# Kernel tuning notes

Measured on AMD Instinct MI355X. Metric: run time of the kernel, lower is better.

Reference implementation:

```python
import jax, jax.numpy as jnp
import numpy as np

D_MODEL = 128; N_HEADS = 8; N_LEVELS = 1; N_POINTS = 8
MAX_RES = 10.0
B, H_SP, W_SP = 8, 64, 64


def setup_inputs() -> dict:
    key = jax.random.key(0)
    ks = jax.random.split(key, 8)
    s = 0.02
    f32 = jnp.float32
    return {
        "nbr_fea": jax.random.normal(ks[0], (B, D_MODEL, H_SP, W_SP), f32),
        "ext_fea": jax.random.normal(ks[1], (B, D_MODEL, H_SP, W_SP), f32),
        "W_val": jax.random.normal(ks[2], (D_MODEL, D_MODEL), f32) * s,
        "b_val": jnp.zeros((D_MODEL,), f32),
        "W_off": jax.random.normal(ks[3], (D_MODEL, N_HEADS * N_LEVELS * N_POINTS * 2), f32) * s,
        "b_off": jax.random.normal(ks[4], (N_HEADS * N_LEVELS * N_POINTS * 2,), f32) * s,
        "W_attn": jax.random.normal(ks[5], (D_MODEL, N_HEADS * N_LEVELS * N_POINTS), f32) * s,
        "b_attn": jnp.zeros((N_HEADS * N_LEVELS * N_POINTS,), f32),
        "W_out": jax.random.normal(ks[6], (D_MODEL, D_MODEL), f32) * s,
        "b_out": jnp.zeros((D_MODEL,), f32),
    }


def _deform_attn_align(nbr_fea, ext_fea, W_val, b_val, W_off, b_off, W_attn, b_attn, W_out, b_out):
    b, c, h, w = nbr_fea.shape
    L = h * w
    dh = c // N_HEADS
    # flatten b c h w -> b (h w) c
    query = jnp.transpose(ext_fea, (0, 2, 3, 1)).reshape(b, L, c)
    vin = jnp.transpose(nbr_fea, (0, 2, 3, 1)).reshape(b, L, c)

    # value projection (mask is all-False -> no masked fill needed)
    value = (vin @ W_val + b_val).reshape(b, L, N_HEADS, dh)
    vh = jnp.transpose(value, (0, 2, 1, 3))  # [b, H, L, dh]

    # sampling offsets, clamped by max_residue_magnitude * tanh
    off = MAX_RES * jnp.tanh(query @ W_off + b_off)
    off = off.reshape(b, L, N_HEADS, N_POINTS, 2)  # single level
    attn = jax.nn.softmax((query @ W_attn + b_attn).reshape(b, L, N_HEADS, N_POINTS), axis=-1)

    # reference points in [0,1]; valid_ratio == 1 since padding mask is all-False
    yy, xx = jnp.meshgrid(jnp.arange(h, dtype=jnp.float32), jnp.arange(w, dtype=jnp.float32), indexing="ij")
    ref = jnp.stack([(xx.reshape(-1) + 0.5) / w, (yy.reshape(-1) + 0.5) / h], axis=-1)  # [L, 2]
    norm = jnp.array([w, h], jnp.float32)  # offset_normalizer [W, H]
    loc = ref[None, :, None, None, :] + off / norm  # [b, L, H, P, 2]

    # grid_sample(align_corners=False, padding_mode='zeros') pixel coordinates
    px = jnp.transpose(loc[..., 0] * w - 0.5, (0, 2, 1, 3))  # [b, H, L, P]
    py = jnp.transpose(loc[..., 1] * h - 0.5, (0, 2, 1, 3))

    x0 = jnp.floor(px); y0 = jnp.floor(py)
    fx = px - x0; fy = py - y0
    x0i = x0.astype(jnp.int32); y0i = y0.astype(jnp.int32)

    def gather(xi, yi):
        valid = (xi >= 0) & (xi < w) & (yi >= 0) & (yi < h)
        idx = jnp.clip(yi, 0, h - 1) * w + jnp.clip(xi, 0, w - 1)  # [b, H, L, P]
        g = jnp.take_along_axis(vh, idx.reshape(b, N_HEADS, L * N_POINTS)[..., None], axis=2)
        return g.reshape(b, N_HEADS, L, N_POINTS, dh) * valid[..., None]

    samp = (gather(x0i, y0i) * ((1.0 - fx) * (1.0 - fy))[..., None]
            + gather(x0i + 1, y0i) * (fx * (1.0 - fy))[..., None]
            + gather(x0i, y0i + 1) * ((1.0 - fx) * fy)[..., None]
            + gather(x0i + 1, y0i + 1) * (fx * fy)[..., None])  # [b, H, L, P, dh]

    aw = jnp.transpose(attn, (0, 2, 1, 3))  # [b, H, L, P]
    out = jnp.sum(samp * aw[..., None], axis=3)  # [b, H, L, dh]
    out = jnp.transpose(out, (0, 2, 1, 3)).reshape(b, L, c)
    out = out @ W_out + b_out
    return jnp.transpose(out.reshape(b, h, w, c), (0, 3, 1, 2))  # b c h w


def reference(nbr_fea, ext_fea, W_val, b_val, W_off, b_off, W_attn, b_attn, W_out, b_out):
    return _deform_attn_align(nbr_fea, ext_fea, W_val, b_val, W_off, b_off, W_attn, b_attn, W_out, b_out)
```

## Files before the change

kernel.cpp:

```cpp
#include <hip/hip_runtime.h>
#include <cstdint>

#define HB 8
#define CM 128
#define NHEAD 8
#define NPT 8
#define DHD 16
#define HS 64
#define WS 64
#define LTOT 4096
#define NQA 192
#define QAP 196
#define LFP 132
#define WPP 33

typedef float floatx4 __attribute__((ext_vector_type(4)));
typedef short bf16x8 __attribute__((ext_vector_type(8)));

__device__ __forceinline__ unsigned short f2bf_rne(float x) {
  unsigned u = __float_as_uint(x);
  return (unsigned short)((u + 0x7FFFu + ((u >> 16) & 1)) >> 16);
}
__device__ __forceinline__ void split_bf(float x, unsigned short& h, unsigned short& l) {
  unsigned u = __float_as_uint(x);
  h = (unsigned short)(u >> 16);
  float r = x - __uint_as_float(u & 0xFFFF0000u);
  l = (unsigned short)(__float_as_uint(r) >> 16);
}
__device__ __forceinline__ float fast_tanh(float x) {
  float e = __expf(2.0f * x);
  return 1.0f - 2.0f / (e + 1.0f);
}
__device__ __forceinline__ void bf8_fma(floatx4& oa, floatx4& ob, const uint4 r, const float wc) {
  floatx4 va = {__uint_as_float(r.x << 16), __uint_as_float(r.x & 0xFFFF0000u),
                __uint_as_float(r.y << 16), __uint_as_float(r.y & 0xFFFF0000u)};
  floatx4 vb = {__uint_as_float(r.z << 16), __uint_as_float(r.z & 0xFFFF0000u),
                __uint_as_float(r.w << 16), __uint_as_float(r.w & 0xFFFF0000u)};
  oa += va * wc;
  ob += vb * wc;
}

__global__ __launch_bounds__(256) void prep(const float* __restrict__ Wv,
                                            const float* __restrict__ Wo,
                                            const float* __restrict__ Wa,
                                            const float* __restrict__ Ww,
                                            const float* __restrict__ bo,
                                            const float* __restrict__ ba,
                                            unsigned short* __restrict__ wf_val,
                                            unsigned short* __restrict__ wf_qa,
                                            unsigned short* __restrict__ wf_out,
                                            float* __restrict__ bias_qa) {
  const int gid = blockIdx.x * 256 + threadIdx.x;
  const int k4 = gid / 448;
  const int ng = gid - k4 * 448;

  const float* src;
  unsigned short* dst;
  int Nsrc, Nn, nd, n;
  if (ng < 128) {        src = Wv; dst = wf_val; Nsrc = 128; Nn = 128; n = ng;        nd = n; }
  else if (ng < 256) {   src = Wo; dst = wf_qa;  Nsrc = 128; Nn = 192; n = ng - 128;  nd = n; }
  else if (ng < 320) {   src = Wa; dst = wf_qa;  Nsrc = 64;  Nn = 192; n = ng - 256;  nd = n + 128; }
  else {                 src = Ww; dst = wf_out; Nsrc = 128; Nn = 128; n = ng - 320;  nd = n; }

  ushort4 hi, lo;
  split_bf(src[(k4 * 4 + 0) * Nsrc + n], hi.x, lo.x);
  split_bf(src[(k4 * 4 + 1) * Nsrc + n], hi.y, lo.y);
  split_bf(src[(k4 * 4 + 2) * Nsrc + n], hi.z, lo.z);
  split_bf(src[(k4 * 4 + 3) * Nsrc + n], hi.w, lo.w);
  const int off = (k4 >> 1) * Nn * 8 + nd * 8 + (k4 & 1) * 4;
  *(ushort4*)(dst + off) = hi;
  *(ushort4*)(dst + Nn * 128 + off) = lo;

  if (gid < 128) bias_qa[gid] = bo[gid];
  else if (gid < 192) bias_qa[gid] = ba[gid - 128];
}

__global__ __launch_bounds__(256, 4) void gemm_val(const float* __restrict__ nbr,
                                                   const unsigned short* __restrict__ WF,
                                                   const float* __restrict__ bias,
                                                   unsigned short* __restrict__ value) {
  __shared__ __align__(16) char smem[33792];
  unsigned short* AB = (unsigned short*)smem;
  const int t = threadIdx.x;
  const int ml0 = blockIdx.x * 64;
  const int b = blockIdx.y;

  {
    const float* src = nbr + (size_t)b * CM * LTOT + ml0;
    const int x = t & 63, kq = t >> 6;
#pragma unroll
    for (int i = 0; i < 8; i++) {
      const int kb = kq * 4 + i * 16;
      ushort4 hi, lo;
      split_bf(src[(size_t)(kb + 0) * LTOT + x], hi.x, lo.x);
      split_bf(src[(size_t)(kb + 1) * LTOT + x], hi.y, lo.y);
      split_bf(src[(size_t)(kb + 2) * LTOT + x], hi.z, lo.z);
      split_bf(src[(size_t)(kb + 3) * LTOT + x], hi.w, lo.w);
      const int off = x * 128 + (((kb >> 3) ^ (x & 15)) << 3) + (kb & 7);
      *(ushort4*)(AB + off) = hi;
      *(ushort4*)(AB + 8192 + off) = lo;
    }
  }
  __syncthreads();

  const int w = t >> 6, lane = t & 63;
  const int wm = (w >> 1) * 32, wn = (w & 1) * 64;
  const int nl = lane & 15, q = lane >> 4;

  floatx4 acc[2][4];
#pragma unroll
  for (int mt = 0; mt < 2; mt++)
#pragma unroll
    for (int j = 0; j < 4; j++) acc[mt][j] = {0.0f, 0.0f, 0.0f, 0.0f};

#pragma unroll
  for (int K0 = 0; K0 < 4; K0++) {
    bf16x8 ah[2], al[2];
#pragma unroll
    for (int mt = 0; mt < 2; mt++) {
      const int m = wm + mt * 16 + nl;
      const int off = m * 128 + (((K0 * 4 + q) ^ (m & 15)) << 3);
      ah[mt] = *(bf16x8*)(AB + off);
      al[mt] = *(bf16x8*)(AB + 8192 + off);
    }
#pragma unroll
    for (int j = 0; j < 4; j++) {
      const size_t o = (size_t)(K0 * 4 + q) * CM * 8 + (wn + j * 16 + nl) * 8;
      const bf16x8 wh = *(const bf16x8*)(WF + o);
      const bf16x8 wl = *(const bf16x8*)(WF + (size_t)CM * 128 + o);
#pragma unroll
      for (int mt = 0; mt < 2; mt++) {
        acc[mt][j] = __builtin_amdgcn_mfma_f32_16x16x32_bf16(al[mt], wh, acc[mt][j], 0, 0, 0);
        acc[mt][j] = __builtin_amdgcn_mfma_f32_16x16x32_bf16(ah[mt], wl, acc[mt][j], 0, 0, 0);
        acc[mt][j] = __builtin_amdgcn_mfma_f32_16x16x32_bf16(ah[mt], wh, acc[mt][j], 0, 0, 0);
      }
    }
  }

  __syncthreads();
  float* LF = (float*)smem;
#pragma unroll
  for (int j = 0; j < 4; j++) {
    const int gc = wn + j * 16 + nl;
    const float bv = bias[gc];
#pragma unroll
    for (int mt = 0; mt < 2; mt++)
#pragma unroll
      for (int r = 0; r < 4; r++)
        LF[(wm + mt * 16 + q * 4 + r) * LFP + gc] = acc[mt][j][r] + bv;
  }
  __syncthreads();
#pragma unroll
  for (int i = 0; i < 4; i++) {
    const int c = t + i * 256;
    const int h = c >> 7, rem = c & 127, l = rem >> 1, half = rem & 1;
    const float* sp = LF + l * LFP + h * 16 + half * 8;
    uint4 st;
    st.x = ((unsigned)f2bf_rne(sp[1]) << 16) | f2bf_rne(sp[0]);
    st.y = ((unsigned)f2bf_rne(sp[3]) << 16) | f2bf_rne(sp[2]);
    st.z = ((unsigned)f2bf_rne(sp[5]) << 16) | f2bf_rne(sp[4]);
    st.w = ((unsigned)f2bf_rne(sp[7]) << 16) | f2bf_rne(sp[6]);
    *(uint4*)(value + ((size_t)(b * NHEAD + h) * LTOT + ml0 + l) * DHD + half * 8) = st;
  }
}

__global__ __launch_bounds__(256, 2) void samp(const float* __restrict__ ext,
                                               const unsigned short* __restrict__ value,
                                               const unsigned short* __restrict__ wf_qa,
                                               const unsigned short* __restrict__ wf_out,
                                               const float* __restrict__ bias_qa,
                                               const float* __restrict__ b_out,
                                               float* __restrict__ out) {
  __shared__ __align__(16) char smem[33792];
  unsigned short* AB = (unsigned short*)smem;
  float* qaT = (float*)smem;
  float2* WXY = (float2*)smem;
  float* WA = (float*)(smem + 16896);
  unsigned short* FR = (unsigned short*)(smem + 25344);

  const int t = threadIdx.x;
  const int b = blockIdx.x & 7;
  const int ml0 = (blockIdx.x >> 3) * 32;
  const int w = t >> 6, lane = t & 63;
  const int nl = lane & 15, q = lane >> 4;

  {
    const float* src = ext + (size_t)b * CM * LTOT + ml0;
    const int x = t & 31, kq = t >> 5;
#pragma unroll
    for (int i = 0; i < 4; i++) {
      const int kb = i * 32 + kq * 4;
      ushort4 hi, lo;
      split_bf(src[(size_t)(kb + 0) * LTOT + x], hi.x, lo.x);
      split_bf(src[(size_t)(kb + 1) * LTOT + x], hi.y, lo.y);
      split_bf(src[(size_t)(kb + 2) * LTOT + x], hi.z, lo.z);
      split_bf(src[(size_t)(kb + 3) * LTOT + x], hi.w, lo.w);
      const int off = x * 128 + (((kb >> 3) ^ (x & 15)) << 3) + (kb & 7);
      *(ushort4*)(AB + off) = hi;
      *(ushort4*)(AB + 4096 + off) = lo;
    }
  }
  __syncthreads();

  {
    const int wm = (w & 1) * 16;
    const int wn = (w >> 1) * 96;
    floatx4 acc[6];
#pragma unroll
    for (int j = 0; j < 6; j++) acc[j] = {0.0f, 0.0f, 0.0f, 0.0f};
#pragma unroll
    for (int K0 = 0; K0 < 4; K0++) {
      const int m = wm + nl;
      const int off = m * 128 + (((K0 * 4 + q) ^ (m & 15)) << 3);
      const bf16x8 ah = *(bf16x8*)(AB + off);
      const bf16x8 al = *(bf16x8*)(AB + 4096 + off);
#pragma unroll
      for (int j = 0; j < 6; j++) {
        const size_t o = (size_t)(K0 * 4 + q) * NQA * 8 + (wn + j * 16 + nl) * 8;
        const bf16x8 wh = *(const bf16x8*)(wf_qa + o);
        const bf16x8 wl = *(const bf16x8*)(wf_qa + (size_t)NQA * 128 + o);
        acc[j] = __builtin_amdgcn_mfma_f32_16x16x32_bf16(al, wh, acc[j], 0, 0, 0);
        acc[j] = __builtin_amdgcn_mfma_f32_16x16x32_bf16(ah, wl, acc[j], 0, 0, 0);
        acc[j] = __builtin_amdgcn_mfma_f32_16x16x32_bf16(ah, wh, acc[j], 0, 0, 0);
      }
    }
    __syncthreads();
#pragma unroll
    for (int j = 0; j < 6; j++) {
      const int n = wn + j * 16 + nl;
      const float bv = bias_qa[n];
#pragma unroll
      for (int r = 0; r < 4; r++)
        qaT[(wm + q * 4 + r) * QAP + n] = acc[j][r] + bv;
    }
  }
  __syncthreads();

  {
    const int ll = t >> 3, h = t & 7;
    const float* qrow = qaT + ll * QAP;
    float4 of[4];
#pragma unroll
    for (int j = 0; j < 4; j++) of[j] = *(const float4*)(qrow + h * 16 + j * 4);
    const float4 lga = *(const float4*)(qrow + 128 + h * 8);
    const float4 lgb = *(const float4*)(qrow + 128 + h * 8 + 4);
    __syncthreads();
    const float lg[8] = {lga.x, lga.y, lga.z, lga.w, lgb.x, lgb.y, lgb.z, lgb.w};
    float m = lg[0];
#pragma unroll
    for (int p = 1; p < 8; p++) m = fmaxf(m, lg[p]);
    float e[8], s = 0.0f;
#pragma unroll
    for (int p = 0; p < 8; p++) { e[p] = __expf(lg[p] - m); s += e[p]; }
    const float inv = 1.0f / s;
    const int l = ml0 + ll;
    const float xf = (float)(l & (WS - 1));
    const float yf = (float)(l >> 6);
#pragma unroll
    for (int p = 0; p < 8; p++) {
      const float ox = (p & 1) ? of[p >> 1].z : of[p >> 1].x;
      const float oy = (p & 1) ? of[p >> 1].w : of[p >> 1].y;
      WXY[(h * 8 + p) * WPP + ll] = {xf + 10.0f * fast_tanh(ox), yf + 10.0f * fast_tanh(oy)};
      WA[(h * 8 + p) * WPP + ll] = e[p] * inv;
    }
  }
  __syncthreads();

  {
    const int llq = lane >> 1, half = lane & 1;
    const int llm = llq & 15;
#pragma unroll
    for (int hi2 = 0; hi2 < 2; hi2++) {
      const int hh = w + hi2 * 4;
      const unsigned short* vb = value + (size_t)(b * NHEAD + hh) * LTOT * DHD + half * 8;
      floatx4 oa = {0.f, 0.f, 0.f, 0.f}, ob = oa;
#pragma unroll
      for (int p = 0; p < 8; p++) {
        const float2 pxy = WXY[(hh * 8 + p) * WPP + llq];
        const float a = WA[(hh * 8 + p) * WPP + llq];
        const float x0f = floorf(pxy.x), y0f = floorf(pxy.y);
        const float fx = pxy.x - x0f, fy = pxy.y - y0f;
        const int ix = (int)x0f, iy = (int)y0f;
        float wc[4];
        unsigned adr[4];
#pragma unroll
        for (int c = 0; c < 4; c++) {
          const int cdx = c & 1, cdy = c >> 1;
          const int jx = ix + cdx, jy = iy + cdy;
          const float wx = cdx ? fx : 1.0f - fx;
          const float wy = cdy ? fy : 1.0f - fy;
          const bool valid = ((unsigned)jx < WS) & ((unsigned)jy < HS);
          wc[c] = valid ? a * wx * wy : 0.0f;
          const int cx = min(max(jx, 0), WS - 1);
          const int cy = min(max(jy, 0), HS - 1);
          adr[c] = (unsigned)((cy << 6) + cx) * DHD;
        }
        uint4 r[4];
#pragma unroll
        for (int c = 0; c < 4; c++) r[c] = *(const uint4*)(vb + adr[c]);
#pragma unroll
        for (int c = 0; c < 4; c++) bf8_fma(oa, ob, r[c], wc[c]);
      }
      const int off = llq * 128 + (((hh * 2 + half) ^ llm) << 3);
      uint4 st;
      st.x = ((unsigned)f2bf_rne(oa[1]) << 16) | f2bf_rne(oa[0]);
      st.y = ((unsigned)f2bf_rne(oa[3]) << 16) | f2bf_rne(oa[2]);
      st.z = ((unsigned)f2bf_rne(ob[1]) << 16) | f2bf_rne(ob[0]);
      st.w = ((unsigned)f2bf_rne(ob[3]) << 16) | f2bf_rne(ob[2]);
      *(uint4*)(FR + off) = st;
    }
  }
  __syncthreads();

  {
    const int wm = (w & 1) * 16;
    const int wn = (w >> 1) * 64;
    floatx4 acc[4];
#pragma unroll
    for (int j = 0; j < 4; j++) acc[j] = {0.0f, 0.0f, 0.0f, 0.0f};
#pragma unroll
    for (int K0 = 0; K0 < 4; K0++) {
      const int m = wm + nl;
      const int off = m * 128 + (((K0 * 4 + q) ^ (m & 15)) << 3);
      const bf16x8 ah = *(bf16x8*)(FR + off);
#pragma unroll
      for (int j = 0; j < 4; j++) {
        const int n = wn + j * 16 + nl;
        const size_t o = (size_t)(K0 * 4 + q) * CM * 8 + n * 8;
        const bf16x8 wh = *(const bf16x8*)(wf_out + o);
        const bf16x8 wl = *(const bf16x8*)(wf_out + (size_t)CM * 128 + o);
        acc[j] = __builtin_amdgcn_mfma_f32_16x16x32_bf16(ah, wl, acc[j], 0, 0, 0);
        acc[j] = __builtin_amdgcn_mfma_f32_16x16x32_bf16(ah, wh, acc[j], 0, 0, 0);
      }
    }
#pragma unroll
    for (int j = 0; j < 4; j++) {
      const int gc = wn + j * 16 + nl;
      const float bv = b_out[gc];
      float4 st = {acc[j][0] + bv, acc[j][1] + bv, acc[j][2] + bv, acc[j][3] + bv};
      *(float4*)(out + ((size_t)b * CM + gc) * LTOT + ml0 + wm + q * 4) = st;
    }
  }
}

extern "C" void kernel_launch(void* const* d_in, const int* in_sizes, int n_in,
                              void* d_out, int out_size, void* d_ws, size_t ws_size,
                              hipStream_t stream) {
  const float* nbr    = (const float*)d_in[0];
  const float* ext    = (const float*)d_in[1];
  const float* W_val  = (const float*)d_in[2];
  const float* b_val  = (const float*)d_in[3];
  const float* W_off  = (const float*)d_in[4];
  const float* b_off  = (const float*)d_in[5];
  const float* W_attn = (const float*)d_in[6];
  const float* b_attn = (const float*)d_in[7];
  const float* W_out  = (const float*)d_in[8];
  const float* b_out  = (const float*)d_in[9];
  float* out = (float*)d_out;

  unsigned short* value = (unsigned short*)d_ws;
  unsigned short* wf_val = value + (size_t)HB * NHEAD * LTOT * DHD;
  unsigned short* wf_qa  = wf_val + 128 * 128 * 2;
  unsigned short* wf_out = wf_qa + 192 * 128 * 2;
  float* bias_qa = (float*)(wf_out + 128 * 128 * 2);

  prep<<<56, 256, 0, stream>>>(W_val, W_off, W_attn, W_out, b_off, b_attn,
                               wf_val, wf_qa, wf_out, bias_qa);
  gemm_val<<<dim3(64, HB), 256, 0, stream>>>(nbr, wf_val, b_val, value);
  samp<<<dim3(128 * HB), 256, 0, stream>>>(ext, value, wf_qa, wf_out, bias_qa, b_out, out);
}
```

Baseline: 136.6 us.

## Move query projection into the value-projection kernel and slim the sampling kernel

The offset/attention projection, tanh and softmax move out of the sampling kernel into a combined projection kernel. That kernel runs 1024 value-projection blocks (now 32 rows each) alongside 1024 query-projection blocks. Sampling positions and weights are packed to a global buffer, so the sampling kernel needs only 8 KB of shared memory and can target occupancy 4 instead of 2. The cost is an extra global round trip of about 24 floats per (position, head), roughly 25 MB written and read back.

New measurement: 152.2 us. +11.4%, slower.

```diff
diff --git a/kernel.cpp b/kernel.cpp
--- a/kernel.cpp
+++ b/kernel.cpp
@@ -12,7 +12,6 @@
 #define NQA 192
 #define QAP 196
 #define LFP 132
-#define WPP 33
 
 typedef float floatx4 __attribute__((ext_vector_type(4)));
 typedef short bf16x8 __attribute__((ext_vector_type(8)));
@@ -75,108 +74,188 @@
   else if (gid < 192) bias_qa[gid] = ba[gid - 128];
 }
 
-__global__ __launch_bounds__(256, 4) void gemm_val(const float* __restrict__ nbr,
-                                                   const unsigned short* __restrict__ WF,
-                                                   const float* __restrict__ bias,
-                                                   unsigned short* __restrict__ value) {
-  __shared__ __align__(16) char smem[33792];
-  unsigned short* AB = (unsigned short*)smem;
+__global__ __launch_bounds__(256, 4) void proj(const float* __restrict__ nbr,
+                                               const float* __restrict__ ext,
+                                               const unsigned short* __restrict__ wf_val,
+                                               const float* __restrict__ b_val,
+                                               const unsigned short* __restrict__ wf_qa,
+                                               const float* __restrict__ bias_qa,
+                                               unsigned short* __restrict__ value,
+                                               float* __restrict__ wpack) {
+  __shared__ __align__(16) char smem[25088];
   const int t = threadIdx.x;
-  const int ml0 = blockIdx.x * 64;
-  const int b = blockIdx.y;
-
-  {
-    const float* src = nbr + (size_t)b * CM * LTOT + ml0;
-    const int x = t & 63, kq = t >> 6;
-#pragma unroll
-    for (int i = 0; i < 8; i++) {
-      const int kb = kq * 4 + i * 16;
-      ushort4 hi, lo;
-      split_bf(src[(size_t)(kb + 0) * LTOT + x], hi.x, lo.x);
-      split_bf(src[(size_t)(kb + 1) * LTOT + x], hi.y, lo.y);
-      split_bf(src[(size_t)(kb + 2) * LTOT + x], hi.z, lo.z);
-      split_bf(src[(size_t)(kb + 3) * LTOT + x], hi.w, lo.w);
-      const int off = x * 128 + (((kb >> 3) ^ (x & 15)) << 3) + (kb & 7);
-      *(ushort4*)(AB + off) = hi;
-      *(ushort4*)(AB + 8192 + off) = lo;
+  const int w = t >> 6, lane = t & 63;
+  const int nl = lane & 15, q = lane >> 4;
+
+  if (blockIdx.x < 1024) {
+    const int bx = blockIdx.x;
+    const int b = bx >> 7;
+    const int ml0 = (bx & 127) * 32;
+    unsigned short* AB = (unsigned short*)smem;
+    {
+      const float* src = nbr + (size_t)b * CM * LTOT + ml0;
+      const int x = t & 31, kq = t >> 5;
+#pragma unroll
+      for (int i = 0; i < 4; i++) {
+        const int kb = i * 32 + kq * 4;
+        ushort4 hi, lo;
+        split_bf(src[(size_t)(kb + 0) * LTOT + x], hi.x, lo.x);
+        split_bf(src[(size_t)(kb + 1) * LTOT + x], hi.y, lo.y);
+        split_bf(src[(size_t)(kb + 2) * LTOT + x], hi.z, lo.z);
+        split_bf(src[(size_t)(kb + 3) * LTOT + x], hi.w, lo.w);
+        const int off = x * 128 + (((kb >> 3) ^ (x & 15)) << 3) + (kb & 7);
+        *(ushort4*)(AB + off) = hi;
+        *(ushort4*)(AB + 4096 + off) = lo;
+      }
+    }
+    __syncthreads();
+
+    const int wm = (w & 1) * 16, wn = (w >> 1) * 64;
+    floatx4 acc[4];
+#pragma unroll
+    for (int j = 0; j < 4; j++) acc[j] = {0.0f, 0.0f, 0.0f, 0.0f};
+
+#pragma unroll
+    for (int K0 = 0; K0 < 4; K0++) {
+      const int m = wm + nl;
+      const int off = m * 128 + (((K0 * 4 + q) ^ (m & 15)) << 3);
+      const bf16x8 ah = *(bf16x8*)(AB + off);
+      const bf16x8 al = *(bf16x8*)(AB + 4096 + off);
+#pragma unroll
+      for (int j = 0; j < 4; j++) {
+        const size_t o = (size_t)(K0 * 4 + q) * CM * 8 + (wn + j * 16 + nl) * 8;
+        const bf16x8 wh = *(const bf16x8*)(wf_val + o);
+        const bf16x8 wl = *(const bf16x8*)(wf_val + (size_t)CM * 128 + o);
+        acc[j] = __builtin_amdgcn_mfma_f32_16x16x32_bf16(al, wh, acc[j], 0, 0, 0);
+        acc[j] = __builtin_amdgcn_mfma_f32_16x16x32_bf16(ah, wl, acc[j], 0, 0, 0);
+        acc[j] = __builtin_amdgcn_mfma_f32_16x16x32_bf16(ah, wh, acc[j], 0, 0, 0);
+      }
+    }
+
+    __syncthreads();
+    float* LF = (float*)smem;
+#pragma unroll
+    for (int j = 0; j < 4; j++) {
+      const int gc = wn + j * 16 + nl;
+      const float bv = b_val[gc];
+#pragma unroll
+      for (int r = 0; r < 4; r++)
+        LF[(wm + q * 4 + r) * LFP + gc] = acc[j][r] + bv;
+    }
+    __syncthreads();
+#pragma unroll
+    for (int i = 0; i < 2; i++) {
+      const int c = t + i * 256;
+      const int h = c >> 6, rem = c & 63, l = rem >> 1, half = rem & 1;
+      const float* sp = LF + l * LFP + h * 16 + half * 8;
+      uint4 st;
+      st.x = ((unsigned)f2bf_rne(sp[1]) << 16) | f2bf_rne(sp[0]);
+      st.y = ((unsigned)f2bf_rne(sp[3]) << 16) | f2bf_rne(sp[2]);
+      st.z = ((unsigned)f2bf_rne(sp[5]) << 16) | f2bf_rne(sp[4]);
+      st.w = ((unsigned)f2bf_rne(sp[7]) << 16) | f2bf_rne(sp[6]);
+      *(uint4*)(value + ((size_t)(b * NHEAD + h) * LTOT + ml0 + l) * DHD + half * 8) = st;
+    }
+  } else {
+    const int i0 = blockIdx.x - 1024;
+    const int b = i0 & 7;
+    const int ml0 = (i0 >> 3) * 32;
+    unsigned short* AB = (unsigned short*)smem;
+    float* qaT = (float*)smem;
+    {
+      const float* src = ext + (size_t)b * CM * LTOT + ml0;
+      const int x = t & 31, kq = t >> 5;
+#pragma unroll
+      for (int i = 0; i < 4; i++) {
+        const int kb = i * 32 + kq * 4;
+        ushort4 hi, lo;
+        split_bf(src[(size_t)(kb + 0) * LTOT + x], hi.x, lo.x);
+        split_bf(src[(size_t)(kb + 1) * LTOT + x], hi.y, lo.y);
+        split_bf(src[(size_t)(kb + 2) * LTOT + x], hi.z, lo.z);
+        split_bf(src[(size_t)(kb + 3) * LTOT + x], hi.w, lo.w);
+        const int off = x * 128 + (((kb >> 3) ^ (x & 15)) << 3) + (kb & 7);
+        *(ushort4*)(AB + off) = hi;
+        *(ushort4*)(AB + 4096 + off) = lo;
+      }
+    }
+    __syncthreads();
+
+    {
+      const int wm = (w & 1) * 16;
+      const int wn = (w >> 1) * 96;
+      floatx4 acc[6];
+#pragma unroll
+      for (int j = 0; j < 6; j++) acc[j] = {0.0f, 0.0f, 0.0f, 0.0f};
+#pragma unroll
+      for (int K0 = 0; K0 < 4; K0++) {
+        const int m = wm + nl;
+        const int off = m * 128 + (((K0 * 4 + q) ^ (m & 15)) << 3);
+        const bf16x8 ah = *(bf16x8*)(AB + off);
+        const bf16x8 al = *(bf16x8*)(AB + 4096 + off);
+#pragma unroll
+        for (int j = 0; j < 6; j++) {
+          const size_t o = (size_t)(K0 * 4 + q) * NQA * 8 + (wn + j * 16 + nl) * 8;
+          const bf16x8 wh = *(const bf16x8*)(wf_qa + o);
+          const bf16x8 wl = *(const bf16x8*)(wf_qa + (size_t)NQA * 128 + o);
+          acc[j] = __builtin_amdgcn_mfma_f32_16x16x32_bf16(al, wh, acc[j], 0, 0, 0);
+          acc[j] = __builtin_amdgcn_mfma_f32_16x16x32_bf16(ah, wl, acc[j], 0, 0, 0);
+          acc[j] = __builtin_amdgcn_mfma_f32_16x16x32_bf16(ah, wh, acc[j], 0, 0, 0);
+        }
+      }
+      __syncthreads();
+#pragma unroll
+      for (int j = 0; j < 6; j++) {
+        const int n = wn + j * 16 + nl;
+        const float bv = bias_qa[n];
+#pragma unroll
+        for (int r = 0; r < 4; r++)
+          qaT[(wm + q * 4 + r) * QAP + n] = acc[j][r] + bv;
+      }
+    }
+    __syncthreads();
+
+    {
+      const int ll = t >> 3, h = t & 7;
+      const float* qrow = qaT + ll * QAP;
+      float4 of[4];
+#pragma unroll
+      for (int j = 0; j < 4; j++) of[j] = *(const float4*)(qrow + h * 16 + j * 4);
+      const float4 lga = *(const float4*)(qrow + 128 + h * 8);
+      const float4 lgb = *(const float4*)(qrow + 128 + h * 8 + 4);
+      const float lg[8] = {lga.x, lga.y, lga.z, lga.w, lgb.x, lgb.y, lgb.z, lgb.w};
+      float m = lg[0];
+#pragma unroll
+      for (int p = 1; p < 8; p++) m = fmaxf(m, lg[p]);
+      float e[8], s = 0.0f;
+#pragma unroll
+      for (int p = 0; p < 8; p++) { e[p] = __expf(lg[p] - m); s += e[p]; }
+      const float inv = 1.0f / s;
+      const int l = ml0 + ll;
+      const float xf = (float)(l & (WS - 1));
+      const float yf = (float)(l >> 6);
+      float wpl[24];
+#pragma unroll
+      for (int p = 0; p < 8; p++) {
+        const float ox = (p & 1) ? of[p >> 1].z : of[p >> 1].x;
+        const float oy = (p & 1) ? of[p >> 1].w : of[p >> 1].y;
+        wpl[p * 3 + 0] = xf + 10.0f * fast_tanh(ox);
+        wpl[p * 3 + 1] = yf + 10.0f * fast_tanh(oy);
+        wpl[p * 3 + 2] = e[p] * inv;
+      }
+      float* wp = wpack + ((size_t)(b * LTOT + ml0 + ll) * 8 + h) * 24;
+#pragma unroll
+      for (int j = 0; j < 6; j++)
+        *(float4*)(wp + j * 4) = *(float4*)(wpl + j * 4);
     }
   }
-  __syncthreads();
-
-  const int w = t >> 6, lane = t & 63;
-  const int wm = (w >> 1) * 32, wn = (w & 1) * 64;
-  const int nl = lane & 15, q = lane >> 4;
-
-  floatx4 acc[2][4];
-#pragma unroll
-  for (int mt = 0; mt < 2; mt++)
-#pragma unroll
-    for (int j = 0; j < 4; j++) acc[mt][j] = {0.0f, 0.0f, 0.0f, 0.0f};
-
-#pragma unroll
-  for (int K0 = 0; K0 < 4; K0++) {
-    bf16x8 ah[2], al[2];
-#pragma unroll
-    for (int mt = 0; mt < 2; mt++) {
-      const int m = wm + mt * 16 + nl;
-      const int off = m * 128 + (((K0 * 4 + q) ^ (m & 15)) << 3);
-      ah[mt] = *(bf16x8*)(AB + off);
-      al[mt] = *(bf16x8*)(AB + 8192 + off);
-    }
-#pragma unroll
-    for (int j = 0; j < 4; j++) {
-      const size_t o = (size_t)(K0 * 4 + q) * CM * 8 + (wn + j * 16 + nl) * 8;
-      const bf16x8 wh = *(const bf16x8*)(WF + o);
-      const bf16x8 wl = *(const bf16x8*)(WF + (size_t)CM * 128 + o);
-#pragma unroll
-      for (int mt = 0; mt < 2; mt++) {
-        acc[mt][j] = __builtin_amdgcn_mfma_f32_16x16x32_bf16(al[mt], wh, acc[mt][j], 0, 0, 0);
-        acc[mt][j] = __builtin_amdgcn_mfma_f32_16x16x32_bf16(ah[mt], wl, acc[mt][j], 0, 0, 0);
-        acc[mt][j] = __builtin_amdgcn_mfma_f32_16x16x32_bf16(ah[mt], wh, acc[mt][j], 0, 0, 0);
-      }
-    }
-  }
-
-  __syncthreads();
-  float* LF = (float*)smem;
-#pragma unroll
-  for (int j = 0; j < 4; j++) {
-    const int gc = wn + j * 16 + nl;
-    const float bv = bias[gc];
-#pragma unroll
-    for (int mt = 0; mt < 2; mt++)
-#pragma unroll
-      for (int r = 0; r < 4; r++)
-        LF[(wm + mt * 16 + q * 4 + r) * LFP + gc] = acc[mt][j][r] + bv;
-  }
-  __syncthreads();
-#pragma unroll
-  for (int i = 0; i < 4; i++) {
-    const int c = t + i * 256;
-    const int h = c >> 7, rem = c & 127, l = rem >> 1, half = rem & 1;
-    const float* sp = LF + l * LFP + h * 16 + half * 8;
-    uint4 st;
-    st.x = ((unsigned)f2bf_rne(sp[1]) << 16) | f2bf_rne(sp[0]);
-    st.y = ((unsigned)f2bf_rne(sp[3]) << 16) | f2bf_rne(sp[2]);
-    st.z = ((unsigned)f2bf_rne(sp[5]) << 16) | f2bf_rne(sp[4]);
-    st.w = ((unsigned)f2bf_rne(sp[7]) << 16) | f2bf_rne(sp[6]);
-    *(uint4*)(value + ((size_t)(b * NHEAD + h) * LTOT + ml0 + l) * DHD + half * 8) = st;
-  }
-}
-
-__global__ __launch_bounds__(256, 2) void samp(const float* __restrict__ ext,
-                                               const unsigned short* __restrict__ value,
-                                               const unsigned short* __restrict__ wf_qa,
-                                               const unsigned short* __restrict__ wf_out,
-                                               const float* __restrict__ bias_qa,
-                                               const float* __restrict__ b_out,
-                                               float* __restrict__ out) {
-  __shared__ __align__(16) char smem[33792];
-  unsigned short* AB = (unsigned short*)smem;
-  float* qaT = (float*)smem;
-  float2* WXY = (float2*)smem;
-  float* WA = (float*)(smem + 16896);
-  unsigned short* FR = (unsigned short*)(smem + 25344);
+}
+
+__global__ __launch_bounds__(256, 4) void samp2(const unsigned short* __restrict__ value,
+                                                const float* __restrict__ wpack,
+                                                const unsigned short* __restrict__ wf_out,
+                                                const float* __restrict__ b_out,
+                                                float* __restrict__ out) {
+  __shared__ __align__(16) char smem[8192];
+  unsigned short* FR = (unsigned short*)smem;
 
   const int t = threadIdx.x;
   const int b = blockIdx.x & 7;
@@ -185,101 +264,25 @@
   const int nl = lane & 15, q = lane >> 4;
 
   {
-    const float* src = ext + (size_t)b * CM * LTOT + ml0;
-    const int x = t & 31, kq = t >> 5;
-#pragma unroll
-    for (int i = 0; i < 4; i++) {
-      const int kb = i * 32 + kq * 4;
-      ushort4 hi, lo;
-      split_bf(src[(size_t)(kb + 0) * LTOT + x], hi.x, lo.x);
-      split_bf(src[(size_t)(kb + 1) * LTOT + x], hi.y, lo.y);
-      split_bf(src[(size_t)(kb + 2) * LTOT + x], hi.z, lo.z);
-      split_bf(src[(size_t)(kb + 3) * LTOT + x], hi.w, lo.w);
-      const int off = x * 128 + (((kb >> 3) ^ (x & 15)) << 3) + (kb & 7);
-      *(ushort4*)(AB + off) = hi;
-      *(ushort4*)(AB + 4096 + off) = lo;
-    }
-  }
-  __syncthreads();
-
-  {
-    const int wm = (w & 1) * 16;
-    const int wn = (w >> 1) * 96;
-    floatx4 acc[6];
-#pragma unroll
-    for (int j = 0; j < 6; j++) acc[j] = {0.0f, 0.0f, 0.0f, 0.0f};
-#pragma unroll
-    for (int K0 = 0; K0 < 4; K0++) {
-      const int m = wm + nl;
-      const int off = m * 128 + (((K0 * 4 + q) ^ (m & 15)) << 3);
-      const bf16x8 ah = *(bf16x8*)(AB + off);
-      const bf16x8 al = *(bf16x8*)(AB + 4096 + off);
-#pragma unroll
-      for (int j = 0; j < 6; j++) {
-        const size_t o = (size_t)(K0 * 4 + q) * NQA * 8 + (wn + j * 16 + nl) * 8;
-        const bf16x8 wh = *(const bf16x8*)(wf_qa + o);
-        const bf16x8 wl = *(const bf16x8*)(wf_qa + (size_t)NQA * 128 + o);
-        acc[j] = __builtin_amdgcn_mfma_f32_16x16x32_bf16(al, wh, acc[j], 0, 0, 0);
-        acc[j] = __builtin_amdgcn_mfma_f32_16x16x32_bf16(ah, wl, acc[j], 0, 0, 0);
-        acc[j] = __builtin_amdgcn_mfma_f32_16x16x32_bf16(ah, wh, acc[j], 0, 0, 0);
-      }
-    }
-    __syncthreads();
-#pragma unroll
-    for (int j = 0; j < 6; j++) {
-      const int n = wn + j * 16 + nl;
-      const float bv = bias_qa[n];
-#pragma unroll
-      for (int r = 0; r < 4; r++)
-        qaT[(wm + q * 4 + r) * QAP + n] = acc[j][r] + bv;
-    }
-  }
-  __syncthreads();
-
-  {
-    const int ll = t >> 3, h = t & 7;
-    const float* qrow = qaT + ll * QAP;
-    float4 of[4];
-#pragma unroll
-    for (int j = 0; j < 4; j++) of[j] = *(const float4*)(qrow + h * 16 + j * 4);
-    const float4 lga = *(const float4*)(qrow + 128 + h * 8);
-    const float4 lgb = *(const float4*)(qrow + 128 + h * 8 + 4);
-    __syncthreads();
-    const float lg[8] = {lga.x, lga.y, lga.z, lga.w, lgb.x, lgb.y, lgb.z, lgb.w};
-    float m = lg[0];
-#pragma unroll
-    for (int p = 1; p < 8; p++) m = fmaxf(m, lg[p]);
-    float e[8], s = 0.0f;
-#pragma unroll
-    for (int p = 0; p < 8; p++) { e[p] = __expf(lg[p] - m); s += e[p]; }
-    const float inv = 1.0f / s;
-    const int l = ml0 + ll;
-    const float xf = (float)(l & (WS - 1));
-    const float yf = (float)(l >> 6);
-#pragma unroll
-    for (int p = 0; p < 8; p++) {
-      const float ox = (p & 1) ? of[p >> 1].z : of[p >> 1].x;
-      const float oy = (p & 1) ? of[p >> 1].w : of[p >> 1].y;
-      WXY[(h * 8 + p) * WPP + ll] = {xf + 10.0f * fast_tanh(ox), yf + 10.0f * fast_tanh(oy)};
-      WA[(h * 8 + p) * WPP + ll] = e[p] * inv;
-    }
-  }
-  __syncthreads();
-
-  {
     const int llq = lane >> 1, half = lane & 1;
     const int llm = llq & 15;
 #pragma unroll
     for (int hi2 = 0; hi2 < 2; hi2++) {
       const int hh = w + hi2 * 4;
+      const float* wp = wpack + ((size_t)(b * LTOT + ml0 + llq) * 8 + hh) * 24;
+      float wpl[24];
+#pragma unroll
+      for (int j = 0; j < 6; j++)
+        *(float4*)(wpl + j * 4) = *(const float4*)(wp + j * 4);
       const unsigned short* vb = value + (size_t)(b * NHEAD + hh) * LTOT * DHD + half * 8;
       floatx4 oa = {0.f, 0.f, 0.f, 0.f}, ob = oa;
 #pragma unroll
       for (int p = 0; p < 8; p++) {
-        const float2 pxy = WXY[(hh * 8 + p) * WPP + llq];
-        const float a = WA[(hh * 8 + p) * WPP + llq];
-        const float x0f = floorf(pxy.x), y0f = floorf(pxy.y);
-        const float fx = pxy.x - x0f, fy = pxy.y - y0f;
+        const float pxx = wpl[p * 3 + 0];
+        const float pyy = wpl[p * 3 + 1];
+        const float a = wpl[p * 3 + 2];
+        const float x0f = floorf(pxx), y0f = floorf(pyy);
+        const float fx = pxx - x0f, fy = pyy - y0f;
         const int ix = (int)x0f, iy = (int)y0f;
         float wc[4];
         unsigned adr[4];
@@ -363,9 +366,10 @@
   unsigned short* wf_qa  = wf_val + 128 * 128 * 2;
   unsigned short* wf_out = wf_qa + 192 * 128 * 2;
   float* bias_qa = (float*)(wf_out + 128 * 128 * 2);
+  float* wpack   = bias_qa + 192;
 
   prep<<<56, 256, 0, stream>>>(W_val, W_off, W_attn, W_out, b_off, b_attn,
                                wf_val, wf_qa, wf_out, bias_qa);
-  gemm_val<<<dim3(64, HB), 256, 0, stream>>>(nbr, wf_val, b_val, value);
-  samp<<<dim3(128 * HB), 256, 0, stream>>>(ext, value, wf_qa, wf_out, bias_qa, b_out, out);
-}
+  proj<<<2048, 256, 0, stream>>>(nbr, ext, wf_val, b_val, wf_qa, bias_qa, value, wpack);
+  samp2<<<1024, 256, 0, stream>>>(value, wpack, wf_out, b_out, out);
+}
```
